# Performance work log

Measured on AMD Instinct MI355X. Metric: run time of the kernel, lower is better.

Reference implementation:

```python
import jax, jax.numpy as jnp
import numpy as np

N = 64      # SSM state size (hidden_size)
H = 1024    # channels
L = 2048    # sequence length
BATCH = 8


def setup_inputs() -> dict:
    key = jax.random.key(0)
    ks = jax.random.split(key, 12)
    s = 1.0 / np.sqrt(N)
    n = jnp.arange(N, dtype=jnp.float32)
    return {
        "r": jax.random.normal(ks[0], (BATCH, L, H), dtype=jnp.float32),
        "B_re": jax.random.normal(ks[1], (N,), dtype=jnp.float32) * s,
        "B_im": jax.random.normal(ks[2], (N,), dtype=jnp.float32) * s,
        "C_re": jax.random.normal(ks[3], (H, N), dtype=jnp.float32) * s,
        "C_im": jax.random.normal(ks[4], (H, N), dtype=jnp.float32) * s,
        "P_re": jax.random.normal(ks[5], (N,), dtype=jnp.float32) * s,
        "P_im": jax.random.normal(ks[6], (N,), dtype=jnp.float32) * s,
        "Q_re": jax.random.normal(ks[7], (N,), dtype=jnp.float32) * s,
        "Q_im": jax.random.normal(ks[8], (N,), dtype=jnp.float32) * s,
        # HiPPO-LegS-like diagonal: negative real part for stability, imag ~ pi*n
        "diag_re": -0.5 * jnp.ones((N,), dtype=jnp.float32),
        "diag_im": jnp.pi * (n - N / 2.0),
        "step": jnp.array([1e-3], dtype=jnp.float32),
        "D": jnp.zeros((1,), dtype=jnp.float32),
    }


def _dplr_kernel(Bc, Cc, Pc, Qc, Lam, step, seq_len):
    # Standard S4 DPLR generating function evaluated at roots of unity,
    # then inverse FFT -> real convolution kernel K_c of shape (H, L).
    z = jnp.exp(-2j * jnp.pi * jnp.arange(seq_len) / seq_len).astype(jnp.complex64)  # (L,)
    g = (2.0 / step) * (1.0 - z) / (1.0 + z)                                          # (L,)
    cden = 1.0 / (g[:, None] - Lam[None, :])                                          # (L,N) Cauchy denom
    k00 = jnp.einsum('hn,ln->hl', Cc * Bc, cden)   # (H,L)
    k01 = jnp.einsum('hn,ln->hl', Cc * Pc, cden)   # (H,L)
    k10 = jnp.einsum('n,ln->l', Qc * Bc, cden)     # (L,)
    k11 = jnp.einsum('n,ln->l', Qc * Pc, cden)     # (L,)
    at_roots = (2.0 / (1.0 + z)) * (k00 - k01 * (k10 / (1.0 + k11)))  # (H,L)
    return jnp.fft.ifft(at_roots, axis=-1).real


def reference(r, B_re, B_im, C_re, C_im, P_re, P_im, Q_re, Q_im,
              diag_re, diag_im, step, D):
    step_c = jnp.maximum(step[0], 1e-6)
    Bc = B_re + 1j * B_im
    Cc = C_re + 1j * C_im
    Pc = P_re + 1j * P_im
    Qc = Q_re + 1j * Q_im
    Lam = diag_re + 1j * diag_im
    seq_len = r.shape[1]
    K = _dplr_kernel(Bc, Cc, Pc, Qc, Lam, step_c, seq_len)  # (H, L)
    # causal FFT convolution along the sequence axis
    nfft = 2 * seq_len
    Kf = jnp.fft.rfft(K, n=nfft, axis=-1)            # (H, nfft//2+1)
    uf = jnp.fft.rfft(r, n=nfft, axis=1)             # (B, nfft//2+1, H)
    h1 = jnp.fft.irfft(uf * Kf.T[None], n=nfft, axis=1)[:, :seq_len]  # (B,L,H)
    y1 = h1 + D[0] * r
    return jax.nn.gelu(y1, approximate=False)
```

## Files before the change

kernel.cpp:

```cpp
#include <hip/hip_runtime.h>
#include <math.h>

#define SSM_N 64
#define SSM_H 1024
#define SSM_L 2048
#define SSM_B 8
#define FFTN 2048
#define NT 256
#define KFS 2052

#define PSWZ(a) ((a) ^ (((a) >> 4) & 15))

typedef float f2 __attribute__((ext_vector_type(2)));
static __device__ __forceinline__ f2 mkf2(float a, float b){ f2 v; v.x = a; v.y = b; return v; }

static __device__ __forceinline__ f2 cmul(f2 a, f2 b){
  return mkf2(-a.y, a.y) * mkf2(b.y, b.x) + mkf2(a.x, a.x) * b;
}
static __device__ __forceinline__ f2 cconj(f2 a){ return mkf2(a.x, -a.y); }

template<bool INV> static __device__ __forceinline__ f2 mul_mi(f2 a){
  return INV ? mkf2(-a.y, a.x) : mkf2(a.y, -a.x);
}
template<bool INV> static __device__ __forceinline__ f2 mul_w81(f2 a){
  const float r = 0.70710678118654752440f;
  return INV ? (r * mkf2(a.x - a.y, a.y + a.x)) : (r * mkf2(a.x + a.y, a.y - a.x));
}
template<bool INV> static __device__ __forceinline__ f2 mul_w83(f2 a){
  const float r = 0.70710678118654752440f;
  return INV ? (r * mkf2(-(a.x + a.y), a.x - a.y)) : (r * mkf2(a.y - a.x, -(a.x + a.y)));
}

#define W8C0 1.f
#define W8S0 0.f
#define W8C1 0.92387953251f
#define W8S1 (-0.38268343236f)
#define W8C2 0.70710678119f
#define W8S2 (-0.70710678119f)
#define W8C3 0.38268343236f
#define W8S3 (-0.92387953251f)
#define W8C4 0.f
#define W8S4 (-1.f)
#define W8C5 (-0.38268343236f)
#define W8S5 (-0.92387953251f)
#define W8C6 (-0.70710678119f)
#define W8S6 (-0.70710678119f)
#define W8C7 (-0.92387953251f)
#define W8S7 (-0.38268343236f)

template<bool INV>
static __device__ __forceinline__ void bfly8_store(f2* __restrict__ dst, const f2* __restrict__ tw,
                                                   f2* x, int j, int base, int S)
{
  f2 t0=x[0]+x[4], t4=x[0]-x[4];
  f2 t1=x[1]+x[5], t5=x[1]-x[5];
  f2 t2=x[2]+x[6], t6=x[2]-x[6];
  f2 t3=x[3]+x[7], t7=x[3]-x[7];
  f2 b0=t0+t2, b2=t0-t2, b1=t1+t3, b3=t1-t3;
  f2 mb3 = mul_mi<INV>(b3);
  f2 y0=b0+b1, y4=b0-b1, y2=b2+mb3, y6=b2-mb3;
  f2 v1 = mul_w81<INV>(t5), v2 = mul_mi<INV>(t6), v3 = mul_w83<INV>(t7);
  f2 a0=t4+v2, a2=t4-v2, a1=v1+v3, a3=v1-v3;
  f2 ma3 = mul_mi<INV>(a3);
  f2 y1=a0+a1, y5=a0-a1, y3=a2+ma3, y7=a2-ma3;
  f2 w1 = tw[j];
  if (INV) w1.y = -w1.y;
  f2 w2 = cmul(w1,w1);
  f2 w3 = cmul(w2,w1);
  f2 w4 = cmul(w2,w2);
  f2 w5 = cmul(w3,w2);
  f2 w6 = cmul(w3,w3);
  f2 w7 = cmul(w4,w3);
  dst[PSWZ(base)]     = y0;
  dst[PSWZ(base+S)]   = cmul(y1,w1);
  dst[PSWZ(base+2*S)] = cmul(y2,w2);
  dst[PSWZ(base+3*S)] = cmul(y3,w3);
  dst[PSWZ(base+4*S)] = cmul(y4,w4);
  dst[PSWZ(base+5*S)] = cmul(y5,w5);
  dst[PSWZ(base+6*S)] = cmul(y6,w6);
  dst[PSWZ(base+7*S)] = cmul(y7,w7);
}

template<bool INV, bool ZTOP>
static __device__ __forceinline__ void stage8_first(const f2* __restrict__ src, f2* __restrict__ dst,
                                                    const f2* __restrict__ tw, int t, int st)
{
  const f2* sp = src + st;
  f2 x[8];
  if (ZTOP) {
    #pragma unroll
    for (int q = 0; q < 4; ++q) { x[q] = sp[256*q]; x[q+4] = mkf2(0.f, 0.f); }
  } else {
    #pragma unroll
    for (int q = 0; q < 8; ++q) x[q] = sp[256*q];
  }
  bfly8_store<INV>(dst, tw, x, t, t*8, 1);
}

template<bool INV, int S>
static __device__ __forceinline__ void stage8_mid(const f2* __restrict__ src, f2* __restrict__ dst,
                                                  const f2* __restrict__ tw, int t, int st)
{
  const f2* sp = src + st;
  f2 x[8];
  #pragma unroll
  for (int q = 0; q < 8; ++q) x[q] = sp[256*q];
  int i = t & (S-1);
  int j = t - i;
  bfly8_store<INV>(dst, tw, x, j, i + j*8, S);
}

template<bool INV, bool HALFOUT>
static __device__ __forceinline__ void stage4f(const f2* __restrict__ src, f2* __restrict__ dst, int st)
{
  #pragma unroll
  for (int hh = 0; hh < 2; ++hh) {
    const f2* sp = src + st + 256*hh;
    f2* wp = dst + st + 256*hh;
    f2 x0=sp[0], x1=sp[512], x2=sp[1024], x3=sp[1536];
    f2 a0=x0+x2, a2=x0-x2, a1=x1+x3, a3=x1-x3;
    f2 m = mul_mi<INV>(a3);
    wp[0]   = a0+a1;
    wp[512] = a2+m;
    if (!HALFOUT) {
      wp[1024] = a0-a1;
      wp[1536] = a2-m;
    }
  }
}

template<bool INV, bool ZTOP, bool HALFOUT>
static __device__ void fft2048(f2* A, f2* B, const f2* tw, int t, int st)
{
  __syncthreads();
  stage8_first<INV, ZTOP>(A, B, tw, t, st);
  __syncthreads();
  stage8_mid<INV, 8>(B, A, tw, t, st);
  __syncthreads();
  stage8_mid<INV, 64>(A, B, tw, t, st);
  __syncthreads();
  stage4f<INV, HALFOUT>(B, A, st);
  __syncthreads();
}

static __device__ __forceinline__ void init_tw(f2* tw, int t)
{
  float s, c;
  sincosf(-6.2831853071795864769f * (float)t / (float)FFTN, &s, &c);
  tw[t] = mkf2(c, s);
}

__global__ __launch_bounds__(256) void kprep(
    const float* __restrict__ r, float* __restrict__ rT,
    const float* __restrict__ B_re, const float* __restrict__ B_im,
    const float* __restrict__ P_re, const float* __restrict__ P_im,
    const float* __restrict__ Q_re, const float* __restrict__ Q_im,
    const float* __restrict__ diag_re, const float* __restrict__ diag_im,
    const float* __restrict__ step,
    f2* __restrict__ cdenT, f2* __restrict__ f2v, f2* __restrict__ facv)
{
  __shared__ float til[64][65];
  int bid = blockIdx.x;
  int t = threadIdx.x;
  if (bid < 4096) {
    int tx = t & 15, ty = t >> 4;
    int h0 = (bid & 15) * 64, l0 = ((bid >> 4) & 31) * 64, b = bid >> 9;
    const float4* s4 = (const float4*)(r + ((size_t)b*SSM_L + l0)*SSM_H + h0);
    #pragma unroll
    for (int i = 0; i < 4; ++i) {
      int lr = ty + 16*i;
      float4 v = s4[(size_t)lr*(SSM_H/4) + tx];
      til[lr][4*tx+0]=v.x; til[lr][4*tx+1]=v.y; til[lr][4*tx+2]=v.z; til[lr][4*tx+3]=v.w;
    }
    __syncthreads();
    float4* d4 = (float4*)(rT + ((size_t)b*SSM_H + h0)*SSM_L + l0);
    #pragma unroll
    for (int i = 0; i < 4; ++i) {
      int hr = ty + 16*i;
      float4 w;
      w.x = til[4*tx+0][hr]; w.y = til[4*tx+1][hr];
      w.z = til[4*tx+2][hr]; w.w = til[4*tx+3][hr];
      d4[(size_t)hr*(SSM_L/4) + tx] = w;
    }
  } else {
    int gid = (bid - 4096) * 256 + t;
    int l = gid >> 3, s = gid & 7;
    double stepc = (double)step[0]; if (stepc < 1e-6) stepc = 1e-6;
    double ang = -2.0 * 3.14159265358979323846 * (double)l / (double)SSM_L;
    double zr = cos(ang), zi = sin(ang);
    double dr = 1.0 + zr, di = zi;
    double nr = 1.0 - zr, ni = -zi;
    double den = dr*dr + di*di;
    double i2s = 2.0 / stepc;
    double gr = i2s * (nr*dr + ni*di) / den;
    double gi = i2s * (ni*dr - nr*di) / den;
    double k10r=0.0, k10i=0.0, k11r=0.0, k11i=0.0;
    #pragma unroll
    for (int q = 0; q < 8; ++q) {
      int n = s*8 + q;
      double ar = gr - (double)diag_re[n];
      double ai = gi - (double)diag_im[n];
      double d2 = ar*ar + ai*ai;
      double cr = ar/d2, ci = -ai/d2;
      cdenT[n*SSM_L + l] = mkf2((float)cr, (float)ci);
      double qr = (double)Q_re[n], qi = (double)Q_im[n];
      double br = (double)B_re[n], bi = (double)B_im[n];
      double pr = (double)P_re[n], pi = (double)P_im[n];
      double qbr = qr*br - qi*bi, qbi = qr*bi + qi*br;
      double qpr = qr*pr - qi*pi, qpi = qr*pi + qi*pr;
      k10r += qbr*cr - qbi*ci; k10i += qbr*ci + qbi*cr;
      k11r += qpr*cr - qpi*ci; k11i += qpr*ci + qpi*cr;
    }
    #pragma unroll
    for (int off = 1; off < 8; off <<= 1) {
      k10r += __shfl_xor(k10r, off);
      k10i += __shfl_xor(k10i, off);
      k11r += __shfl_xor(k11r, off);
      k11i += __shfl_xor(k11i, off);
    }
    if (s == 0) {
      f2v[l] = mkf2((float)(2.0*dr/den), (float)(-2.0*di/den));
      double er = 1.0 + k11r, ei = k11i;
      double ed = er*er + ei*ei;
      facv[l] = mkf2((float)((k10r*er + k10i*ei)/ed), (float)((k10i*er - k10r*ei)/ed));
    }
  }
}

__global__ __launch_bounds__(NT, 2) void kkern(
    const float* __restrict__ C_re, const float* __restrict__ C_im,
    const float* __restrict__ B_re, const float* __restrict__ B_im,
    const float* __restrict__ P_re, const float* __restrict__ P_im,
    const f2* __restrict__ cdenT, const f2* __restrict__ f2v, const f2* __restrict__ facv,
    f2* __restrict__ Kf)
{
  __shared__ f2 bufA[FFTN];
  __shared__ f2 bufB[FFTN];
  __shared__ f2 tw[256];
  int t = threadIdx.x, st = PSWZ(t);
  int h0 = blockIdx.x * 2;
  init_tw(tw, t);
  f2* cbs = bufA;
  if (t < 128) {
    int h = h0 + (t >> 6), n = t & 63;
    f2 cc = mkf2(C_re[h*SSM_N + n], C_im[h*SSM_N + n]);
    cbs[t]       = cmul(cc, mkf2(B_re[n], B_im[n]));
    cbs[128 + t] = cmul(cc, mkf2(P_re[n], P_im[n]));
  }
  __syncthreads();
  f2 k00[2][8], k01[2][8];
  #pragma unroll
  for (int h = 0; h < 2; ++h)
    #pragma unroll
    for (int i = 0; i < 8; ++i) { k00[h][i] = mkf2(0.f,0.f); k01[h][i] = mkf2(0.f,0.f); }
  for (int n = 0; n < SSM_N; ++n) {
    f2 cd[8];
    #pragma unroll
    for (int i = 0; i < 8; ++i) cd[i] = cdenT[n*SSM_L + t + i*NT];
    #pragma unroll
    for (int h = 0; h < 2; ++h) {
      f2 cb = cbs[h*64 + n], cp = cbs[128 + h*64 + n];
      #pragma unroll
      for (int i = 0; i < 8; ++i) {
        k00[h][i] = k00[h][i] + cmul(cb, cd[i]);
        k01[h][i] = k01[h][i] + cmul(cp, cd[i]);
      }
    }
  }
  const float Wc8[8] = {W8C0,W8C1,W8C2,W8C3,W8C4,W8C5,W8C6,W8C7};
  const float Ws8[8] = {W8S0,W8S1,W8S2,W8S3,W8S4,W8S5,W8S6,W8S7};
  float sb, cb2;
  sincosf(-3.14159265358979f * (float)t / (float)FFTN, &sb, &cb2);
  f2 cbase = mkf2(cb2, sb);
  for (int hh = 0; hh < 2; ++hh) {
    __syncthreads();
    #pragma unroll
    for (int i = 0; i < 8; ++i) {
      int l = t + i*NT;
      f2 fv = f2v[l], fc = facv[l];
      bufA[PSWZ(l)] = cmul(fv, k00[hh][i] - cmul(k01[hh][i], fc));
    }
    __syncthreads();
    f2* krow = Kf + (size_t)(h0 + hh) * KFS;
    #pragma unroll
    for (int i = 0; i < 4; ++i) {
      int m = t + i*NT;
      if (m == 0) {
        krow[0]    = mkf2(bufA[0].x, 0.f);
        krow[FFTN] = mkf2(bufA[PSWZ(FFTN/2)].x, 0.f);
      } else {
        krow[2*m] = 0.5f * (bufA[PSWZ(m)] + cconj(bufA[PSWZ(FFTN - m)]));
      }
    }
    fft2048<true, false, false>(bufA, bufB, tw, t, st);
    const float scale = 1.0f / (float)FFTN;
    #pragma unroll
    for (int i = 0; i < 8; ++i) {
      int n = t + i*NT;
      float K = bufA[PSWZ(n)].x * scale;
      bufA[PSWZ(n)] = K * cmul(cbase, mkf2(Wc8[i], Ws8[i]));
    }
    fft2048<false, false, true>(bufA, bufB, tw, t, st);
    #pragma unroll
    for (int i = 0; i < 4; ++i) {
      int m = t + i*NT;
      krow[2*m+1] = bufA[PSWZ(m)];
    }
  }
}

__global__ __launch_bounds__(NT, 4) void kconv(float* __restrict__ rT, const f2* __restrict__ Kf,
                                               const float* __restrict__ Dp)
{
  __shared__ f2 bufA[FFTN];
  __shared__ f2 bufB[FFTN];
  __shared__ f2 tw[256];
  int t = threadIdx.x, st = PSWZ(t);
  int h = blockIdx.x >> 3;
  int b = blockIdx.x & 7;
  float Dv = Dp[0];
  init_tw(tw, t);
  float* rrow = rT + ((size_t)b*SSM_H + h) * SSM_L;
  const float4* r4 = (const float4*)rrow;
  float4 vin[2];
  #pragma unroll
  for (int i = 0; i < 2; ++i) {
    int j2 = t + i*NT;
    vin[i] = r4[j2];
    bufA[PSWZ(2*j2)]   = mkf2(vin[i].x, vin[i].y);
    bufA[PSWZ(2*j2+1)] = mkf2(vin[i].z, vin[i].w);
  }
  fft2048<false, true, false>(bufA, bufB, tw, t, st);
  const f2* krow = Kf + (size_t)h * KFS;
  float sb, cb;
  sincosf(-3.14159265358979f * (float)t / (float)FFTN, &sb, &cb);
  f2 base = mkf2(cb, sb);
  {
    const float Wc[4] = {W8C0,W8C1,W8C2,W8C3};
    const float Ws[4] = {W8S0,W8S1,W8S2,W8S3};
    #pragma unroll
    for (int i = 0; i < 4; ++i) {
      int k = t + i*NT;
      f2 w = cmul(base, mkf2(Wc[i], Ws[i]));
      float c = w.x, s = w.y;
      if (k == 0) {
        f2 c0 = bufA[0];
        float F0 = c0.x + c0.y, Fn = c0.x - c0.y;
        f2 G0 = F0 * krow[0];
        f2 Gn = Fn * krow[FFTN];
        f2 Xe = 0.5f * (G0 + Gn);
        f2 Xo = 0.5f * (G0 - Gn);
        bufB[0] = mkf2(Xe.x - Xo.y, Xe.y + Xo.x);
        f2 Gm = cmul(cconj(bufA[PSWZ(FFTN/2)]), krow[FFTN/2]);
        bufB[PSWZ(FFTN/2)] = cconj(Gm);
      } else {
        int kk = FFTN - k;
        f2 Ck = bufA[PSWZ(k)], Ckk = bufA[PSWZ(kk)];
        f2 E = mkf2(0.5f*(Ck.x + Ckk.x), 0.5f*(Ck.y - Ckk.y));
        f2 O = mkf2(0.5f*(Ck.y + Ckk.y), 0.5f*(Ckk.x - Ck.x));
        f2 Fk  = E + cmul(mkf2(c, s), O);
        f2 Fkk = cconj(E) + cmul(mkf2(-c, s), cconj(O));
        f2 Gk  = cmul(Fk,  krow[k]);
        f2 Gkk = cmul(Fkk, krow[kk]);
        f2 Xe  = mkf2(0.5f*(Gk.x + Gkk.x), 0.5f*(Gk.y - Gkk.y));
        f2 Dd  = mkf2(0.5f*(Gk.x - Gkk.x), 0.5f*(Gk.y + Gkk.y));
        f2 Xo  = cmul(mkf2(c, -s), Dd);
        bufB[PSWZ(k)] = mkf2(Xe.x - Xo.y, Xe.y + Xo.x);
        f2 Xe2 = mkf2(0.5f*(Gkk.x + Gk.x), 0.5f*(Gkk.y - Gk.y));
        f2 Dd2 = mkf2(0.5f*(Gkk.x - Gk.x), 0.5f*(Gkk.y + Gk.y));
        f2 Xo2 = cmul(mkf2(-c, -s), Dd2);
        bufB[PSWZ(kk)] = mkf2(Xe2.x - Xo2.y, Xe2.y + Xo2.x);
      }
    }
  }
  fft2048<true, false, true>(bufB, bufA, tw, t, st);
  const float sc = 1.0f / (float)FFTN;
  float4* w4 = (float4*)rrow;
  #pragma unroll
  for (int i = 0; i < 2; ++i) {
    int j2 = t + i*NT;
    f2 z0 = bufB[PSWZ(2*j2)], z1 = bufB[PSWZ(2*j2+1)];
    w4[j2] = make_float4(z0.x*sc + Dv*vin[i].x, z0.y*sc + Dv*vin[i].y,
                         z1.x*sc + Dv*vin[i].z, z1.y*sc + Dv*vin[i].w);
  }
}

__global__ __launch_bounds__(256) void ktback(const float* __restrict__ yT, float* __restrict__ out)
{
  __shared__ float til[64][65];
  int t = threadIdx.x, tx = t & 15, ty = t >> 4;
  int h0 = blockIdx.x * 64, l0 = blockIdx.y * 64, b = blockIdx.z;
  const float4* s4 = (const float4*)(yT + ((size_t)b*SSM_H + h0)*SSM_L + l0);
  #pragma unroll
  for (int i = 0; i < 4; ++i) {
    int hr = ty + 16*i;
    float4 v = s4[(size_t)hr*(SSM_L/4) + tx];
    til[hr][4*tx+0]=v.x; til[hr][4*tx+1]=v.y; til[hr][4*tx+2]=v.z; til[hr][4*tx+3]=v.w;
  }
  __syncthreads();
  float4* d4 = (float4*)(out + ((size_t)b*SSM_L + l0)*SSM_H + h0);
  #pragma unroll
  for (int i = 0; i < 4; ++i) {
    int lr = ty + 16*i;
    float4 w;
    float x0 = til[4*tx+0][lr], x1 = til[4*tx+1][lr];
    float x2 = til[4*tx+2][lr], x3 = til[4*tx+3][lr];
    w.x = 0.5f * x0 * (1.0f + erff(x0 * 0.70710678118654752f));
    w.y = 0.5f * x1 * (1.0f + erff(x1 * 0.70710678118654752f));
    w.z = 0.5f * x2 * (1.0f + erff(x2 * 0.70710678118654752f));
    w.w = 0.5f * x3 * (1.0f + erff(x3 * 0.70710678118654752f));
    d4[(size_t)lr*(SSM_H/4) + tx] = w;
  }
}

extern "C" void kernel_launch(void* const* d_in, const int* in_sizes, int n_in,
                              void* d_out, int out_size, void* d_ws, size_t ws_size,
                              hipStream_t stream)
{
  const float* r       = (const float*)d_in[0];
  const float* B_re    = (const float*)d_in[1];
  const float* B_im    = (const float*)d_in[2];
  const float* C_re    = (const float*)d_in[3];
  const float* C_im    = (const float*)d_in[4];
  const float* P_re    = (const float*)d_in[5];
  const float* P_im    = (const float*)d_in[6];
  const float* Q_re    = (const float*)d_in[7];
  const float* Q_im    = (const float*)d_in[8];
  const float* diag_re = (const float*)d_in[9];
  const float* diag_im = (const float*)d_in[10];
  const float* step    = (const float*)d_in[11];
  const float* Dp      = (const float*)d_in[12];
  float* out = (float*)d_out;

  char* p = (char*)d_ws;
  float* rT  = (float*)p; p += (size_t)SSM_B*SSM_H*SSM_L*sizeof(float);
  f2* cdenT  = (f2*)p;    p += (size_t)SSM_N*SSM_L*sizeof(f2);
  f2* f2v    = (f2*)p;    p += (size_t)SSM_L*sizeof(f2);
  f2* facv   = (f2*)p;    p += (size_t)SSM_L*sizeof(f2);
  f2* Kf     = (f2*)p;    p += (size_t)SSM_H*KFS*sizeof(f2);

  kprep<<<4096 + 64, 256, 0, stream>>>(r, rT, B_re, B_im, P_re, P_im, Q_re, Q_im,
                                       diag_re, diag_im, step, cdenT, f2v, facv);
  kkern<<<SSM_H/2, NT, 0, stream>>>(C_re, C_im, B_re, B_im, P_re, P_im,
                                    cdenT, f2v, facv, Kf);
  kconv<<<SSM_B*SSM_H, NT, 0, stream>>>(rT, Kf, Dp);
  ktback<<<dim3(SSM_H/64, SSM_L/64, SSM_B), 256, 0, stream>>>(rT, out);
}
```

Baseline: 271.4 us.

## Fold real-FFT packing into precomputed P/Q filter and prune zero-padded FFT

The kernel-spectrum stage now precomputes per-channel coefficient pairs (P,Q) that fold the real-to-complex pack/unpack twiddles into the filter. The convolution then does a single complex multiply-add per bin instead of the full split/merge step. The forward FFT exploits the zero-padded half of the input in its first radix-8 stage, and the inverse FFT computes only the first half of the outputs in its last stage. Other changes: the cdenT loads are software-prefetched one iteration ahead, and block-to-channel indexing is remapped so blocks sharing a channel spread across XCDs. The cost is a larger precomputed table (float4 per bin) read by every block.

```diff
diff --git a/kernel.cpp b/kernel.cpp
--- a/kernel.cpp
+++ b/kernel.cpp
@@ -7,7 +7,6 @@
 #define SSM_B 8
 #define FFTN 2048
 #define NT 256
-#define KFS 2052
 
 #define PSWZ(a) ((a) ^ (((a) >> 4) & 15))
 
@@ -232,7 +231,7 @@
     const float* __restrict__ B_re, const float* __restrict__ B_im,
     const float* __restrict__ P_re, const float* __restrict__ P_im,
     const f2* __restrict__ cdenT, const f2* __restrict__ f2v, const f2* __restrict__ facv,
-    f2* __restrict__ Kf)
+    float4* __restrict__ PQg)
 {
   __shared__ f2 bufA[FFTN];
   __shared__ f2 bufB[FFTN];
@@ -253,10 +252,13 @@
   for (int h = 0; h < 2; ++h)
     #pragma unroll
     for (int i = 0; i < 8; ++i) { k00[h][i] = mkf2(0.f,0.f); k01[h][i] = mkf2(0.f,0.f); }
+  f2 cd[8];
+  #pragma unroll
+  for (int i = 0; i < 8; ++i) cd[i] = cdenT[t + i*NT];
   for (int n = 0; n < SSM_N; ++n) {
-    f2 cd[8];
-    #pragma unroll
-    for (int i = 0; i < 8; ++i) cd[i] = cdenT[n*SSM_L + t + i*NT];
+    f2 cdn[8];
+    #pragma unroll
+    for (int i = 0; i < 8; ++i) cdn[i] = cdenT[((n+1)&63)*SSM_L + t + i*NT];
     #pragma unroll
     for (int h = 0; h < 2; ++h) {
       f2 cb = cbs[h*64 + n], cp = cbs[128 + h*64 + n];
@@ -266,6 +268,8 @@
         k01[h][i] = k01[h][i] + cmul(cp, cd[i]);
       }
     }
+    #pragma unroll
+    for (int i = 0; i < 8; ++i) cd[i] = cdn[i];
   }
   const float Wc8[8] = {W8C0,W8C1,W8C2,W8C3,W8C4,W8C5,W8C6,W8C7};
   const float Ws8[8] = {W8S0,W8S1,W8S2,W8S3,W8S4,W8S5,W8S6,W8S7};
@@ -281,15 +285,15 @@
       bufA[PSWZ(l)] = cmul(fv, k00[hh][i] - cmul(k01[hh][i], fc));
     }
     __syncthreads();
-    f2* krow = Kf + (size_t)(h0 + hh) * KFS;
+    f2 ebin[4]; f2 e2048 = mkf2(0.f, 0.f);
     #pragma unroll
     for (int i = 0; i < 4; ++i) {
       int m = t + i*NT;
       if (m == 0) {
-        krow[0]    = mkf2(bufA[0].x, 0.f);
-        krow[FFTN] = mkf2(bufA[PSWZ(FFTN/2)].x, 0.f);
+        ebin[i] = mkf2(bufA[0].x, 0.f);
+        e2048   = mkf2(bufA[PSWZ(FFTN/2)].x, 0.f);
       } else {
-        krow[2*m] = 0.5f * (bufA[PSWZ(m)] + cconj(bufA[PSWZ(FFTN - m)]));
+        ebin[i] = 0.5f * (bufA[PSWZ(m)] + cconj(bufA[PSWZ(FFTN - m)]));
       }
     }
     fft2048<true, false, false>(bufA, bufB, tw, t, st);
@@ -302,86 +306,101 @@
     }
     fft2048<false, false, true>(bufA, bufB, tw, t, st);
     #pragma unroll
+    for (int i = 0; i < 4; ++i) bufB[t + i*NT] = ebin[i];
+    if (t == 0) bufB[FFTN/2] = e2048;
+    __syncthreads();
+    float4* pqrow = PQg + (size_t)(h0 + hh) * FFTN;
+    const float q4 = 1.0f / 4096.0f;
+    #pragma unroll
     for (int i = 0; i < 4; ++i) {
       int m = t + i*NT;
-      krow[2*m+1] = bufA[PSWZ(m)];
-    }
-  }
-}
-
-__global__ __launch_bounds__(NT, 4) void kconv(float* __restrict__ rT, const f2* __restrict__ Kf,
+      f2 Ka = bufB[m];
+      f2 Kb = bufB[1024 - m];
+      float sv, cv;
+      sincosf(3.0679615757712824e-3f * (float)m, &sv, &cv);
+      float am = q4*(1.f - sv), ap = q4*(1.f + sv), cq = q4*cv;
+      f2 P = mkf2(Ka.x*am + Kb.x*ap, Ka.y*am - Kb.y*ap);
+      f2 dd = mkf2(Ka.x - Kb.x, Ka.y + Kb.y);
+      pqrow[2*m] = make_float4(P.x, P.y, -dd.y*cq, dd.x*cq);
+    }
+    #pragma unroll
+    for (int i = 0; i < 4; ++i) {
+      int m = t + i*NT;
+      f2 Ka = bufA[PSWZ(m)];
+      f2 Kb = bufA[PSWZ(1023 - m)];
+      float sv, cv;
+      sincosf(1.5339807878856412e-3f * (float)(2*m+1), &sv, &cv);
+      float am = q4*(1.f - sv), ap = q4*(1.f + sv), cq = q4*cv;
+      f2 P = mkf2(Ka.x*am + Kb.x*ap, Ka.y*am - Kb.y*ap);
+      f2 dd = mkf2(Ka.x - Kb.x, Ka.y + Kb.y);
+      pqrow[2*m+1] = make_float4(P.x, P.y, -dd.y*cq, dd.x*cq);
+    }
+  }
+}
+
+__global__ __launch_bounds__(NT, 4) void kconv(float* __restrict__ rT,
+                                               const float4* __restrict__ PQg,
                                                const float* __restrict__ Dp)
 {
   __shared__ f2 bufA[FFTN];
   __shared__ f2 bufB[FFTN];
   __shared__ f2 tw[256];
   int t = threadIdx.x, st = PSWZ(t);
-  int h = blockIdx.x >> 3;
-  int b = blockIdx.x & 7;
+  int xc = blockIdx.x & 7, y = blockIdx.x >> 3;
+  int h = xc * 128 + (y >> 3);
+  int b = y & 7;
   float Dv = Dp[0];
   init_tw(tw, t);
   float* rrow = rT + ((size_t)b*SSM_H + h) * SSM_L;
-  const float4* r4 = (const float4*)rrow;
-  float4 vin[2];
-  #pragma unroll
-  for (int i = 0; i < 2; ++i) {
-    int j2 = t + i*NT;
-    vin[i] = r4[j2];
-    bufA[PSWZ(2*j2)]   = mkf2(vin[i].x, vin[i].y);
-    bufA[PSWZ(2*j2+1)] = mkf2(vin[i].z, vin[i].w);
-  }
-  fft2048<false, true, false>(bufA, bufB, tw, t, st);
-  const f2* krow = Kf + (size_t)h * KFS;
-  float sb, cb;
-  sincosf(-3.14159265358979f * (float)t / (float)FFTN, &sb, &cb);
-  f2 base = mkf2(cb, sb);
+  const f2* r2 = (const f2*)rrow;
+  f2 rv[4];
+  #pragma unroll
+  for (int i = 0; i < 4; ++i) rv[i] = r2[t + i*NT];
   {
-    const float Wc[4] = {W8C0,W8C1,W8C2,W8C3};
-    const float Ws[4] = {W8S0,W8S1,W8S2,W8S3};
-    #pragma unroll
-    for (int i = 0; i < 4; ++i) {
+    f2 xx[8];
+    #pragma unroll
+    for (int q = 0; q < 4; ++q) { xx[q] = rv[q]; xx[q+4] = mkf2(0.f, 0.f); }
+    bfly8_store<false>(bufB, tw, xx, t, t*8, 1);
+  }
+  __syncthreads();
+  stage8_mid<false, 8>(bufB, bufA, tw, t, st);
+  __syncthreads();
+  stage8_mid<false, 64>(bufA, bufB, tw, t, st);
+  __syncthreads();
+  const float4* pqrow = PQg + (size_t)h * FFTN;
+  float4 pq[8];
+  #pragma unroll
+  for (int i = 0; i < 8; ++i) pq[i] = pqrow[t + i*NT];
+  stage4f<false, false>(bufB, bufA, st);
+  __syncthreads();
+  {
+    f2 xx[8];
+    #pragma unroll
+    for (int i = 0; i < 8; ++i) {
       int k = t + i*NT;
-      f2 w = cmul(base, mkf2(Wc[i], Ws[i]));
-      float c = w.x, s = w.y;
-      if (k == 0) {
-        f2 c0 = bufA[0];
-        float F0 = c0.x + c0.y, Fn = c0.x - c0.y;
-        f2 G0 = F0 * krow[0];
-        f2 Gn = Fn * krow[FFTN];
-        f2 Xe = 0.5f * (G0 + Gn);
-        f2 Xo = 0.5f * (G0 - Gn);
-        bufB[0] = mkf2(Xe.x - Xo.y, Xe.y + Xo.x);
-        f2 Gm = cmul(cconj(bufA[PSWZ(FFTN/2)]), krow[FFTN/2]);
-        bufB[PSWZ(FFTN/2)] = cconj(Gm);
-      } else {
-        int kk = FFTN - k;
-        f2 Ck = bufA[PSWZ(k)], Ckk = bufA[PSWZ(kk)];
-        f2 E = mkf2(0.5f*(Ck.x + Ckk.x), 0.5f*(Ck.y - Ckk.y));
-        f2 O = mkf2(0.5f*(Ck.y + Ckk.y), 0.5f*(Ckk.x - Ck.x));
-        f2 Fk  = E + cmul(mkf2(c, s), O);
-        f2 Fkk = cconj(E) + cmul(mkf2(-c, s), cconj(O));
-        f2 Gk  = cmul(Fk,  krow[k]);
-        f2 Gkk = cmul(Fkk, krow[kk]);
-        f2 Xe  = mkf2(0.5f*(Gk.x + Gkk.x), 0.5f*(Gk.y - Gkk.y));
-        f2 Dd  = mkf2(0.5f*(Gk.x - Gkk.x), 0.5f*(Gk.y + Gkk.y));
-        f2 Xo  = cmul(mkf2(c, -s), Dd);
-        bufB[PSWZ(k)] = mkf2(Xe.x - Xo.y, Xe.y + Xo.x);
-        f2 Xe2 = mkf2(0.5f*(Gkk.x + Gk.x), 0.5f*(Gkk.y - Gk.y));
-        f2 Dd2 = mkf2(0.5f*(Gkk.x - Gk.x), 0.5f*(Gkk.y + Gk.y));
-        f2 Xo2 = cmul(mkf2(-c, -s), Dd2);
-        bufB[PSWZ(kk)] = mkf2(Xe2.x - Xo2.y, Xe2.y + Xo2.x);
-      }
-    }
-  }
-  fft2048<true, false, true>(bufB, bufA, tw, t, st);
-  const float sc = 1.0f / (float)FFTN;
-  float4* w4 = (float4*)rrow;
-  #pragma unroll
-  for (int i = 0; i < 2; ++i) {
-    int j2 = t + i*NT;
-    f2 z0 = bufB[PSWZ(2*j2)], z1 = bufB[PSWZ(2*j2+1)];
-    w4[j2] = make_float4(z0.x*sc + Dv*vin[i].x, z0.y*sc + Dv*vin[i].y,
-                         z1.x*sc + Dv*vin[i].z, z1.y*sc + Dv*vin[i].w);
+      int kk = (FFTN - k) & (FFTN - 1);
+      f2 Ck  = bufA[st + i*NT];
+      f2 Ckk = bufA[PSWZ(kk)];
+      xx[i] = cmul(mkf2(pq[i].x, pq[i].y), Ck) + cmul(mkf2(pq[i].z, pq[i].w), cconj(Ckk));
+    }
+    bfly8_store<true>(bufB, tw, xx, t, t*8, 1);
+  }
+  __syncthreads();
+  stage8_mid<true, 8>(bufB, bufA, tw, t, st);
+  __syncthreads();
+  stage8_mid<true, 64>(bufA, bufB, tw, t, st);
+  __syncthreads();
+  f2* o2 = (f2*)rrow;
+  #pragma unroll
+  for (int hh = 0; hh < 2; ++hh) {
+    const f2* sp = bufB + st + 256*hh;
+    f2 x0=sp[0], x1=sp[512], x2=sp[1024], x3=sp[1536];
+    f2 a0=x0+x2, a2=x0-x2, a1=x1+x3, a3=x1-x3;
+    f2 mm = mul_mi<true>(a3);
+    f2 y0 = a0+a1, y1 = a2+mm;
+    f2 rA = rv[hh], rB = rv[hh+2];
+    o2[t + 256*hh]       = mkf2(y0.x + Dv*rA.x, y0.y + Dv*rA.y);
+    o2[t + 256*hh + 512] = mkf2(y1.x + Dv*rB.x, y1.y + Dv*rB.y);
   }
 }
 
@@ -433,16 +452,16 @@
   float* out = (float*)d_out;
 
   char* p = (char*)d_ws;
-  float* rT  = (float*)p; p += (size_t)SSM_B*SSM_H*SSM_L*sizeof(float);
-  f2* cdenT  = (f2*)p;    p += (size_t)SSM_N*SSM_L*sizeof(f2);
-  f2* f2v    = (f2*)p;    p += (size_t)SSM_L*sizeof(f2);
-  f2* facv   = (f2*)p;    p += (size_t)SSM_L*sizeof(f2);
-  f2* Kf     = (f2*)p;    p += (size_t)SSM_H*KFS*sizeof(f2);
+  float* rT  = (float*)p;  p += (size_t)SSM_B*SSM_H*SSM_L*sizeof(float);
+  f2* cdenT  = (f2*)p;     p += (size_t)SSM_N*SSM_L*sizeof(f2);
+  f2* f2v    = (f2*)p;     p += (size_t)SSM_L*sizeof(f2);
+  f2* facv   = (f2*)p;     p += (size_t)SSM_L*sizeof(f2);
+  float4* PQ = (float4*)p; p += (size_t)SSM_H*FFTN*sizeof(float4);
 
   kprep<<<4096 + 64, 256, 0, stream>>>(r, rT, B_re, B_im, P_re, P_im, Q_re, Q_im,
                                        diag_re, diag_im, step, cdenT, f2v, facv);
   kkern<<<SSM_H/2, NT, 0, stream>>>(C_re, C_im, B_re, B_im, P_re, P_im,
-                                    cdenT, f2v, facv, Kf);
-  kconv<<<SSM_B*SSM_H, NT, 0, stream>>>(rT, Kf, Dp);
+                                    cdenT, f2v, facv, PQ);
+  kconv<<<SSM_B*SSM_H, NT, 0, stream>>>(rT, PQ, Dp);
   ktback<<<dim3(SSM_H/64, SSM_L/64, SSM_B), 256, 0, stream>>>(rT, out);
 }
```

Result: no change. 267.0 us (-1.6%).
